# Kernel optimization log

Measured on AMD Instinct MI355X. Metric: run time of the kernel, lower is better.

## Reference

```python
import jax, jax.numpy as jnp
import numpy as np


def setup_inputs() -> dict:
    key = jax.random.key(0)
    kq, kk, kv = jax.random.split(key, 3)
    B, S, D = 4, 4096, 64
    q = jax.random.normal(kq, (B, S, D), dtype=jnp.float32)
    k = jax.random.normal(kk, (B, S, D), dtype=jnp.float32)
    v = jax.random.normal(kv, (B, S, D), dtype=jnp.float32)
    return {"q": q, "k": k, "v": v}


def reference(q, k, v):
    # Faithful math of the original blocked loop:
    #   output_i += exp(Q_i @ K_j^T) @ V_j, summed over all column blocks j
    # which is exactly unnormalized exponential attention:
    #   out = exp(Q K^T) V  (no 1/sqrt(d) scaling, no softmax normalization,
    #   no max-subtraction -- matching the source module's math).
    scores = jnp.einsum("bqd,bkd->bqk", q, k)  # [B, Sq, Sk]
    return jnp.einsum("bqk,bkd->bqd", jnp.exp(scores), v)  # [B, Sq, D]
```

## Files before the change

kernel.cpp:

```cpp
#include <hip/hip_runtime.h>
#include <hip/hip_bf16.h>


typedef short    s16x4 __attribute__((ext_vector_type(4)));
typedef short    s16x8 __attribute__((ext_vector_type(8)));
typedef _Float16 h16x8 __attribute__((ext_vector_type(8)));
typedef float    fx4   __attribute__((ext_vector_type(4)));
typedef float    fx16  __attribute__((ext_vector_type(16)));

constexpr int S = 4096, D = 64, BN = 128;
constexpr int QROWS = 128;
constexpr int TILES = S / BN;
constexpr int HALF_TILES = TILES / 2;
constexpr int TILE_SHORTS  = 16 * 512;
constexpr int BATCH_SHORTS = TILES * TILE_SHORTS;

__device__ __forceinline__ unsigned short f2bf(float x) {
    unsigned u = __float_as_uint(x);
    u = (u + 0x7FFFu + ((u >> 16) & 1u)) >> 16;
    return (unsigned short)u;
}
__device__ __forceinline__ float bf2f(unsigned short h) {
    return __uint_as_float(((unsigned)h) << 16);
}
__device__ __forceinline__ unsigned short f2h(float x) {
    union { _Float16 h; unsigned short s; } u;
    u.h = (_Float16)x;
    return u.s;
}
__device__ __forceinline__ unsigned pack_bf16(float lo, float hi) {
    __hip_bfloat162 r = __float22bfloat162_rn(make_float2(lo, hi));
    union { __hip_bfloat162 b; unsigned u; } c;
    c.b = r;
    return c.u;
}
__device__ __forceinline__ float ex2(float x) {
#if __has_builtin(__builtin_amdgcn_exp2f)
    return __builtin_amdgcn_exp2f(x);
#else
    return exp2f(x);
#endif
}

__global__ __launch_bounds__(256) void prep2(
    const float* __restrict__ k, const float* __restrict__ v,
    unsigned short* __restrict__ kf, unsigned short* __restrict__ vf,
    float* __restrict__ out)
{
    __shared__ unsigned short tile[128 * 72];
    const int tid   = threadIdx.x;
    const int which = blockIdx.x & 1;
    const int t     = (blockIdx.x >> 1) & 31;
    const int b     = blockIdx.x >> 6;
    const float* src = (which ? v : k) + ((size_t)b * S + t * BN) * D;

    {
        float4 z = make_float4(0.f, 0.f, 0.f, 0.f);
        float4* oz = (float4*)out + (size_t)blockIdx.x * 1024 + tid;
        #pragma unroll
        for (int i = 0; i < 4; ++i) oz[i * 256] = z;
    }

    #pragma unroll
    for (int i = 0; i < 8; ++i) {
        int f   = i * 256 + tid;
        int row = f >> 4;
        int c4  = (f & 15) << 2;
        float4 x = *(const float4*)(src + row * D + c4);
        s16x4 o;
        if (which) o = (s16x4){(short)f2bf(x.x), (short)f2bf(x.y),
                               (short)f2bf(x.z), (short)f2bf(x.w)};
        else       o = (s16x4){(short)f2h(x.x), (short)f2h(x.y),
                               (short)f2h(x.z), (short)f2h(x.w)};
        *(s16x4*)&tile[row * 72 + c4] = o;
    }
    __syncthreads();

    const int lane = tid & 63;
    unsigned short* dst = (which ? vf : kf) + (size_t)b * BATCH_SHORTS + t * TILE_SHORTS;
    #pragma unroll
    for (int i = 0; i < 4; ++i) {
        int c = (tid >> 6) * 4 + i;
        s16x8 o;
        if (which == 0) {
            int row = (c >> 2) * 32 + (lane & 31);
            int dc  = (c & 3) * 16 + (lane >> 5) * 8;
            o = *(const s16x8*)&tile[row * 72 + dc];
        } else {
            int r0 = (c >> 1) * 16 + (lane >> 5) * 8;
            int dc = (c & 1) * 32 + (lane & 31);
            #pragma unroll
            for (int j = 0; j < 8; ++j) o[j] = (short)tile[(r0 + j) * 72 + dc];
        }
        *(s16x8*)(dst + c * 512 + lane * 8) = o;
    }
}

__global__ __launch_bounds__(512, 2) void attn_main4(
    const float* __restrict__ q, const unsigned short* __restrict__ kf,
    const unsigned short* __restrict__ vf, float* __restrict__ out)
{
    __shared__ unsigned short smem[3 * 2 * TILE_SHORTS];

    const int tid = threadIdx.x, lane = tid & 63, w = tid >> 6;
    const int h = lane >> 5, m5 = lane & 31;
    const int mh = w & 1, kkq = w >> 1;
    const int b = blockIdx.y, q0 = blockIdx.x * QROWS;
    const int kh = blockIdx.z;
    const int t0 = kh * HALF_TILES;

    const unsigned short* kfb = kf + (size_t)b * BATCH_SHORTS;
    const unsigned short* vfb = vf + (size_t)b * BATCH_SHORTS;

    const float LOG2E = 1.4426950408889634f;
    h16x8 qf[2][4];
    #pragma unroll
    for (int mt = 0; mt < 2; ++mt) {
        const float* qrow = q + ((size_t)b * S + q0 + mh * 64 + mt * 32 + m5) * D + h * 8;
        #pragma unroll
        for (int ks = 0; ks < 4; ++ks) {
            float4 a = *(const float4*)(qrow + ks * 16);
            float4 c = *(const float4*)(qrow + ks * 16 + 4);
            qf[mt][ks] = (h16x8){
                (_Float16)(a.x * LOG2E), (_Float16)(a.y * LOG2E),
                (_Float16)(a.z * LOG2E), (_Float16)(a.w * LOG2E),
                (_Float16)(c.x * LOG2E), (_Float16)(c.y * LOG2E),
                (_Float16)(c.z * LOG2E), (_Float16)(c.w * LOG2E)};
        }
    }

    fx16 oacc[2][2] = {};

    auto issue = [&](int t, int bi) {
        unsigned short* base = &smem[bi * 2 * TILE_SHORTS];
        #pragma unroll
        for (int ii = 0; ii < 4; ++ii) {
            int c = (ii & 1) * 8 + w;
            const unsigned short* g = (ii < 2 ? kfb : vfb)
                + (size_t)t * TILE_SHORTS + c * 512 + lane * 8;
            unsigned short* l = base + (ii < 2 ? 0 : TILE_SHORTS) + c * 512 + lane * 8;
            __builtin_amdgcn_global_load_lds(
                (const __attribute__((address_space(1))) unsigned int*)g,
                (__attribute__((address_space(3))) unsigned int*)l, 16, 0, 0);
        }
    };

    issue(t0 + 0, 0);
    issue(t0 + 1, 1);

    for (int i = 0; i < HALF_TILES; ++i) {
        const int bi = i % 3;
        __asm__ volatile("" ::: "memory");
        if (i + 1 < HALF_TILES) {
            __builtin_amdgcn_s_waitcnt(0x0F74);
        } else {
            __builtin_amdgcn_s_waitcnt(0x0F70);
        }
        __builtin_amdgcn_s_barrier();
        __asm__ volatile("" ::: "memory");
        if (i + 2 < HALF_TILES) issue(t0 + i + 2, (i + 2) % 3);

        const unsigned short* kb = &smem[bi * 2 * TILE_SHORTS];
        const unsigned short* vb = kb + TILE_SHORTS;

        fx16 sa[2] = {};
        #pragma unroll
        for (int ks = 0; ks < 4; ++ks) {
            h16x8 a = *(const h16x8*)(kb + (kkq * 4 + ks) * 512 + lane * 8);
            #pragma unroll
            for (int mt = 0; mt < 2; ++mt)
                sa[mt] = __builtin_amdgcn_mfma_f32_32x32x16_f16(a, qf[mt][ks], sa[mt], 0, 0, 0);
        }

        unsigned p01[2][8];
        #pragma unroll
        for (int mt = 0; mt < 2; ++mt)
            #pragma unroll
            for (int rp = 0; rp < 8; ++rp)
                p01[mt][rp] = pack_bf16(ex2(sa[mt][2 * rp]), ex2(sa[mt][2 * rp + 1]));

        union frag { unsigned u[4]; s16x8 v; };
        frag A[2][2];
        #pragma unroll
        for (int mt = 0; mt < 2; ++mt) {
#if __has_builtin(__builtin_amdgcn_permlane32_swap)
            typedef unsigned uix2 __attribute__((ext_vector_type(2)));
            uix2 r0 = __builtin_amdgcn_permlane32_swap(p01[mt][0], p01[mt][2], false, false);
            uix2 r1 = __builtin_amdgcn_permlane32_swap(p01[mt][1], p01[mt][3], false, false);
            A[mt][0].u[0] = r0.x; A[mt][0].u[1] = r1.x;
            A[mt][0].u[2] = r0.y; A[mt][0].u[3] = r1.y;
            uix2 r2 = __builtin_amdgcn_permlane32_swap(p01[mt][4], p01[mt][6], false, false);
            uix2 r3 = __builtin_amdgcn_permlane32_swap(p01[mt][5], p01[mt][7], false, false);
            A[mt][1].u[0] = r2.x; A[mt][1].u[1] = r3.x;
            A[mt][1].u[2] = r2.y; A[mt][1].u[3] = r3.y;
#else
            unsigned sw[8];
            #pragma unroll
            for (int rp = 0; rp < 8; ++rp)
                sw[rp] = (unsigned)__shfl_xor((int)p01[mt][rp], 32, 64);
            A[mt][0].u[0] = h ? sw[2]        : p01[mt][0];
            A[mt][0].u[1] = h ? sw[3]        : p01[mt][1];
            A[mt][0].u[2] = h ? p01[mt][2]   : sw[0];
            A[mt][0].u[3] = h ? p01[mt][3]   : sw[1];
            A[mt][1].u[0] = h ? sw[6]        : p01[mt][4];
            A[mt][1].u[1] = h ? sw[7]        : p01[mt][5];
            A[mt][1].u[2] = h ? p01[mt][6]   : sw[4];
            A[mt][1].u[3] = h ? p01[mt][7]   : sw[5];
#endif
        }

        #pragma unroll
        for (int u = 0; u < 2; ++u) {
            int ss = kkq * 2 + u;
            #pragma unroll
            for (int dt = 0; dt < 2; ++dt) {
                s16x8 vv = *(const s16x8*)(vb + (ss * 2 + dt) * 512 + lane * 8);
                #pragma unroll
                for (int mt = 0; mt < 2; ++mt)
                    oacc[mt][dt] = __builtin_amdgcn_mfma_f32_32x32x16_bf16(
                        A[mt][u].v, vv, oacc[mt][dt], 0, 0, 0);
            }
        }
    }

    __syncthreads();
    float* scratch = (float*)smem;
    float* ob = out + (size_t)b * S * D;
    #pragma unroll
    for (int dt = 0; dt < 2; ++dt) {
        if (kkq > 0) {
            float* dst = scratch + (size_t)(mh * 3 + (kkq - 1)) * 2048;
            #pragma unroll
            for (int mt = 0; mt < 2; ++mt)
                #pragma unroll
                for (int r = 0; r < 16; ++r)
                    dst[(mt * 16 + r) * 64 + lane] = oacc[mt][dt][r];
        }
        __syncthreads();
        if (kkq == 0) {
            #pragma unroll
            for (int mt = 0; mt < 2; ++mt)
                #pragma unroll
                for (int r = 0; r < 16; ++r) {
                    float val = oacc[mt][dt][r];
                    #pragma unroll
                    for (int p = 0; p < 3; ++p)
                        val += scratch[(size_t)(mh * 3 + p) * 2048 + (mt * 16 + r) * 64 + lane];
                    int row = q0 + mh * 64 + mt * 32 + (r & 3) + 8 * (r >> 2) + 4 * h;
                    atomicAdd(&ob[(size_t)row * D + dt * 32 + m5], val);
                }
        }
        __syncthreads();
    }
}

__global__ __launch_bounds__(1024) void attn_fallback(
    const float* __restrict__ q, const float* __restrict__ k,
    const float* __restrict__ v, float* __restrict__ out)
{
    __shared__ unsigned short Kh[64][72];
    __shared__ unsigned short Kl[64][72];
    __shared__ unsigned short Vt[64][68];
    __shared__ unsigned short Pf[64][72];

    const int tid = threadIdx.x, lane = tid & 63, wave = tid >> 6;
    const int quad = lane >> 4, tq = lane & 15;
    const int kkb = wave & 3, mba = wave >> 2;
    const int b = blockIdx.y, q0 = blockIdx.x * 64;
    const float* qb = q + (size_t)b * S * D;
    const float* kb = k + (size_t)b * S * D;
    const float* vb = v + (size_t)b * S * D;
    float* ob = out + (size_t)b * S * D;

    s16x8 qh[2], ql[2];
    {
        const float* qrow = qb + (size_t)(q0 + mba * 16 + tq) * D;
        #pragma unroll
        for (int ks = 0; ks < 2; ++ks) {
            const float* src = qrow + ks * 32 + quad * 8;
            float4 f0 = *(const float4*)src;
            float4 f1 = *(const float4*)(src + 4);
            float f[8] = {f0.x, f0.y, f0.z, f0.w, f1.x, f1.y, f1.z, f1.w};
            #pragma unroll
            for (int j = 0; j < 8; ++j) {
                unsigned short hh = f2bf(f[j]);
                qh[ks][j] = (short)hh;
                ql[ks][j] = (short)f2bf(f[j] - bf2f(hh));
            }
        }
    }
    fx4 oacc = {0.f, 0.f, 0.f, 0.f};
    const int krow = tid >> 4, kc4 = (tid & 15) << 2;
    const int vd = tid & 63, vk = (tid >> 6) << 2;

    for (int t = 0; t < S / 64; ++t) {
        __syncthreads();
        const float* kt = kb + (size_t)(t * 64 + krow) * D;
        const float* vt = vb + (size_t)(t * 64 + vk) * D;
        {
            float4 kv = *(const float4*)(kt + kc4);
            unsigned short h0 = f2bf(kv.x), h1 = f2bf(kv.y), h2 = f2bf(kv.z), h3 = f2bf(kv.w);
            s16x4 a = {(short)h0, (short)h1, (short)h2, (short)h3};
            s16x4 l4 = {(short)f2bf(kv.x - bf2f(h0)), (short)f2bf(kv.y - bf2f(h1)),
                        (short)f2bf(kv.z - bf2f(h2)), (short)f2bf(kv.w - bf2f(h3))};
            *(s16x4*)&Kh[krow][kc4] = a;
            *(s16x4*)&Kl[krow][kc4] = l4;
            const float* vs = vt + vd;
            s16x4 vv = {(short)f2bf(vs[0]), (short)f2bf(vs[D]),
                        (short)f2bf(vs[2 * D]), (short)f2bf(vs[3 * D])};
            *(s16x4*)&Vt[vd][vk] = vv;
        }
        __syncthreads();
        fx4 sacc = {0.f, 0.f, 0.f, 0.f};
        #pragma unroll
        for (int ks = 0; ks < 2; ++ks) {
            s16x8 kah = *(const s16x8*)&Kh[kkb * 16 + tq][ks * 32 + quad * 8];
            s16x8 kal = *(const s16x8*)&Kl[kkb * 16 + tq][ks * 32 + quad * 8];
            sacc = __builtin_amdgcn_mfma_f32_16x16x32_bf16(kah, qh[ks], sacc, 0, 0, 0);
            sacc = __builtin_amdgcn_mfma_f32_16x16x32_bf16(kah, ql[ks], sacc, 0, 0, 0);
            sacc = __builtin_amdgcn_mfma_f32_16x16x32_bf16(kal, qh[ks], sacc, 0, 0, 0);
        }
        s16x4 pp = {(short)f2bf(__expf(sacc[0])), (short)f2bf(__expf(sacc[1])),
                    (short)f2bf(__expf(sacc[2])), (short)f2bf(__expf(sacc[3]))};
        *(s16x4*)&Pf[mba * 16 + tq][kkb * 16 + (quad << 2)] = pp;
        __syncthreads();
        #pragma unroll
        for (int ks = 0; ks < 2; ++ks) {
            s16x8 pa = *(const s16x8*)&Pf[mba * 16 + tq][ks * 32 + quad * 8];
            const unsigned short* vr = &Vt[kkb * 16 + tq][ks * 32 + quad * 8];
            s16x4 va = *(const s16x4*)vr;
            s16x4 vb2 = *(const s16x4*)(vr + 4);
            s16x8 vfull = __builtin_shufflevector(va, vb2, 0, 1, 2, 3, 4, 5, 6, 7);
            oacc = __builtin_amdgcn_mfma_f32_16x16x32_bf16(pa, vfull, oacc, 0, 0, 0);
        }
    }
    #pragma unroll
    for (int r = 0; r < 4; ++r)
        ob[(size_t)(q0 + mba * 16 + quad * 4 + r) * D + kkb * 16 + tq] = oacc[r];
}

extern "C" void kernel_launch(void* const* d_in, const int* in_sizes, int n_in,
                              void* d_out, int out_size, void* d_ws, size_t ws_size,
                              hipStream_t stream) {
    const float* q = (const float*)d_in[0];
    const float* k = (const float*)d_in[1];
    const float* v = (const float*)d_in[2];
    float* out = (float*)d_out;
    const int nbatch = in_sizes[0] / (S * D);
    const size_t elems = (size_t)nbatch * S * D;

    const size_t need = elems * 2 * 2;
    if (nbatch == 4 && ws_size >= need && d_ws != nullptr) {
        unsigned short* kf = (unsigned short*)d_ws;
        unsigned short* vf = kf + elems;

        prep2<<<nbatch * TILES * 2, 256, 0, stream>>>(k, v, kf, vf, out);
        dim3 grid(S / QROWS, nbatch, 2);
        attn_main4<<<grid, 512, 0, stream>>>(q, kf, vf, out);
    } else {
        dim3 grid(S / 64, nbatch);
        attn_fallback<<<grid, 1024, 0, stream>>>(q, k, v, out);
    }
}
```

Measured before the change: 93.96 us.

## Replace atomic split-K accumulation with partial buffers and a reduce kernel

```diff
diff --git a/kernel.cpp b/kernel.cpp
--- a/kernel.cpp
+++ b/kernel.cpp
@@ -44,8 +44,7 @@
 
 __global__ __launch_bounds__(256) void prep2(
     const float* __restrict__ k, const float* __restrict__ v,
-    unsigned short* __restrict__ kf, unsigned short* __restrict__ vf,
-    float* __restrict__ out)
+    unsigned short* __restrict__ kf, unsigned short* __restrict__ vf)
 {
     __shared__ unsigned short tile[128 * 72];
     const int tid   = threadIdx.x;
@@ -53,13 +52,6 @@
     const int t     = (blockIdx.x >> 1) & 31;
     const int b     = blockIdx.x >> 6;
     const float* src = (which ? v : k) + ((size_t)b * S + t * BN) * D;
-
-    {
-        float4 z = make_float4(0.f, 0.f, 0.f, 0.f);
-        float4* oz = (float4*)out + (size_t)blockIdx.x * 1024 + tid;
-        #pragma unroll
-        for (int i = 0; i < 4; ++i) oz[i * 256] = z;
-    }
 
     #pragma unroll
     for (int i = 0; i < 8; ++i) {
@@ -98,15 +90,18 @@
 
 __global__ __launch_bounds__(512, 2) void attn_main4(
     const float* __restrict__ q, const unsigned short* __restrict__ kf,
-    const unsigned short* __restrict__ vf, float* __restrict__ out)
+    const unsigned short* __restrict__ vf, float* __restrict__ partial)
 {
     __shared__ unsigned short smem[3 * 2 * TILE_SHORTS];
 
     const int tid = threadIdx.x, lane = tid & 63, w = tid >> 6;
     const int h = lane >> 5, m5 = lane & 31;
     const int mh = w & 1, kkq = w >> 1;
-    const int b = blockIdx.y, q0 = blockIdx.x * QROWS;
-    const int kh = blockIdx.z;
+    const int bid = blockIdx.x;
+    const int slice = bid & 7;
+    const int b = slice >> 1;
+    const int kh = slice & 1;
+    const int q0 = (bid >> 3) * QROWS;
     const int t0 = kh * HALF_TILES;
 
     const unsigned short* kfb = kf + (size_t)b * BATCH_SHORTS;
@@ -225,7 +220,7 @@
 
     __syncthreads();
     float* scratch = (float*)smem;
-    float* ob = out + (size_t)b * S * D;
+    float* pout = partial + ((size_t)kh * 4 + b) * S * D;
     #pragma unroll
     for (int dt = 0; dt < 2; ++dt) {
         if (kkq > 0) {
@@ -247,10 +242,21 @@
                     for (int p = 0; p < 3; ++p)
                         val += scratch[(size_t)(mh * 3 + p) * 2048 + (mt * 16 + r) * 64 + lane];
                     int row = q0 + mh * 64 + mt * 32 + (r & 3) + 8 * (r >> 2) + 4 * h;
-                    atomicAdd(&ob[(size_t)row * D + dt * 32 + m5], val);
+                    pout[(size_t)row * D + dt * 32 + m5] = val;
                 }
         }
         __syncthreads();
+    }
+}
+
+__global__ __launch_bounds__(256) void reduce_out(
+    const float4* __restrict__ p0, const float4* __restrict__ p1,
+    float4* __restrict__ o, int n4)
+{
+    int i = blockIdx.x * 256 + threadIdx.x;
+    if (i < n4) {
+        float4 a = p0[i], b = p1[i];
+        o[i] = make_float4(a.x + b.x, a.y + b.y, a.z + b.z, a.w + b.w);
     }
 }
 
@@ -349,14 +355,18 @@
     const int nbatch = in_sizes[0] / (S * D);
     const size_t elems = (size_t)nbatch * S * D;
 
-    const size_t need = elems * 2 * 2;
+    const size_t need = elems * 2 * 2 + elems * 2 * 4;
     if (nbatch == 4 && ws_size >= need && d_ws != nullptr) {
         unsigned short* kf = (unsigned short*)d_ws;
         unsigned short* vf = kf + elems;
-
-        prep2<<<nbatch * TILES * 2, 256, 0, stream>>>(k, v, kf, vf, out);
-        dim3 grid(S / QROWS, nbatch, 2);
-        attn_main4<<<grid, 512, 0, stream>>>(q, kf, vf, out);
+        float* partial = (float*)(vf + elems);
+
+        prep2<<<nbatch * TILES * 2, 256, 0, stream>>>(k, v, kf, vf);
+        attn_main4<<<256, 512, 0, stream>>>(q, kf, vf, partial);
+        const int n4 = (int)(elems / 4);
+        reduce_out<<<(n4 + 255) / 256, 256, 0, stream>>>(
+            (const float4*)partial, (const float4*)(partial + elems),
+            (float4*)out, n4);
     } else {
         dim3 grid(S / 64, nbatch);
         attn_fallback<<<grid, 1024, 0, stream>>>(q, k, v, out);
```

New measurement: 95.96 us. 1.02x slower.
